# Kernel optimization log

Measured on AMD Instinct MI355X. Metric: run time of the kernel, lower is better.

## Reference

```python
import jax, jax.numpy as jnp
import numpy as np

NUM_ANCHORS = 3
NUM_CLASSES = 80


def setup_inputs() -> dict:
    key = jax.random.key(0)
    k1, _ = jax.random.split(key)
    B, C, G0, G1 = 16, NUM_ANCHORS * (NUM_CLASSES + 5), 64, 64
    x = jax.random.normal(k1, (B, C, G0, G1), dtype=jnp.float32)
    # normalized (w, h) anchor pairs, as in __init__
    anchors = jnp.array([[0.28, 0.22], [0.38, 0.48], [0.90, 0.78]], dtype=jnp.float32)
    return {"x": x, "anchors": anchors}


def reference(x, anchors):
    B = x.shape[0]
    A, nC = NUM_ANCHORS, NUM_CLASSES
    g0, g1 = x.shape[2], x.shape[3]
    # [B, A, g0, g1, 5+nC]
    pred = x.reshape(B, A, nC + 5, g0, g1).transpose(0, 1, 3, 4, 2)

    sx = jax.nn.sigmoid(pred[..., 0])
    sy = jax.nn.sigmoid(pred[..., 1])
    w = pred[..., 2]
    h = pred[..., 3]
    pred_conf = jax.nn.sigmoid(pred[..., 4])
    pred_cls = jax.nn.sigmoid(pred[..., 5:])

    # grid_x varies along axis 2 (row index), grid_y along axis 3 (col index),
    # matching the torch repeat/.t() construction in compute_grid_offsets.
    grid_x = jnp.arange(g0, dtype=x.dtype).reshape(1, 1, g0, 1)
    grid_y = jnp.arange(g1, dtype=x.dtype).reshape(1, 1, 1, g1)
    anchor_w = (anchors[:, 0] * g0).reshape(1, A, 1, 1)
    anchor_h = (anchors[:, 1] * g1).reshape(1, A, 1, 1)

    pred_boxes = jnp.stack(
        [
            sx + grid_x,
            sy + grid_y,
            jnp.exp(w) * anchor_w,
            jnp.exp(h) * anchor_h,
        ],
        axis=-1,
    )  # [B, A, g0, g1, 4]

    scale = jnp.array([g0, g1, g0, g1], dtype=x.dtype)
    return pred_boxes / scale, pred_conf, pred_cls
```

## Files before the change

kernel.cpp:

```cpp
#include <hip/hip_runtime.h>
#include <math.h>

#define NB 16
#define NA 3
#define NC 80
#define GS 4096
#define NPOS (NB * NA * GS)
#define STR 84

__device__ __forceinline__ float sigmoidf_(float v) {
    return 1.0f / (1.0f + __expf(-v));
}

__global__ __launch_bounds__(256, 7) void yolo_kernel(const float* __restrict__ x,
                                                      const float* __restrict__ anchors,
                                                      float* __restrict__ out) {
    __shared__ float lds[4][16 * STR];
    const int tid = threadIdx.x;
    const int w   = tid >> 6;
    const int l   = tid & 63;
    const int ba  = blockIdx.x >> 6;
    const int row = blockIdx.x & 63;
    const int s0  = (row << 6) + (w << 4);
    const float* __restrict__ xb = x + (size_t)ba * 85 * GS + s0;
    float* const ldsw = lds[w];

    const int chl = l >> 2;
    const int p4  = l & 3;
    const float* __restrict__ xc = xb + (size_t)(5 + chl) * GS + p4 * 4;

    float4 v[5];
    #pragma unroll
    for (int k = 0; k < 5; ++k)
        v[k] = *reinterpret_cast<const float4*>(xc + (size_t)k * 16 * GS);

    float tx = 0.f, ty = 0.f, tw = 0.f, th = 0.f, tc = 0.f;
    const bool box_lane = (l < 16);
    if (box_lane) {
        tx = xb[0 * GS + l];
        ty = xb[1 * GS + l];
        tw = xb[2 * GS + l];
        th = xb[3 * GS + l];
        tc = xb[4 * GS + l];
    }

    #pragma unroll
    for (int k = 0; k < 5; ++k) {
        #pragma unroll
        for (int j = 0; j < 4; ++j) {
            const float sv = sigmoidf_((&v[k].x)[j]);
            ldsw[(p4 * 4 + j) * STR + k * 16 + chl] = sv;
        }
    }

    if (box_lane) {
        const int p = s0 + l;
        const int t = ba * GS + p;
        const int a = ba % NA;
        float4 box;
        box.x = (sigmoidf_(tx) + (float)(p >> 6)) * (1.0f / 64.0f);
        box.y = (sigmoidf_(ty) + (float)(p & 63)) * (1.0f / 64.0f);
        box.z = __expf(tw) * anchors[a * 2 + 0];
        box.w = __expf(th) * anchors[a * 2 + 1];
        reinterpret_cast<float4*>(out)[t] = box;
        out[(size_t)NPOS * 4 + t] = sigmoidf_(tc);
    }

    float4* __restrict__ out4 =
        reinterpret_cast<float4*>(out + (size_t)NPOS * 5) + (size_t)(ba * GS + s0) * 20;
    #pragma unroll
    for (int k = 0; k < 5; ++k) {
        const int o4 = (k << 6) + l;
        const int o  = o4 << 2;
        const int p  = o / 80;
        const int ch = o - p * 80;
        out4[o4] = *reinterpret_cast<const float4*>(&ldsw[p * STR + ch]);
    }
}

extern "C" void kernel_launch(void* const* d_in, const int* in_sizes, int n_in,
                              void* d_out, int out_size, void* d_ws, size_t ws_size,
                              hipStream_t stream) {
    const float* x       = (const float*)d_in[0];
    const float* anchors = (const float*)d_in[1];
    float* out           = (float*)d_out;
    const int blocks = NB * NA * 64;
    yolo_kernel<<<blocks, 256, 0, stream>>>(x, anchors, out);
}
```

Baseline: 116.1 us.

## Use block-wide 128-position LDS transpose tile with channel-major layout

Each block now handles 128 spatial positions, where previously each wave handled its own 16-position slice. All 256 threads load class channels as float4 rows into a shared channel-major LDS tile padded to 133 floats per row. After a block barrier, the tile is read back position-major as scalar gathers and written out as float4. The grid shrinks by half and per-thread loads double. In exchange it adds a __syncthreads, and the minimum-occupancy hint in the launch bounds is dropped.

```diff
diff --git a/kernel.cpp b/kernel.cpp
--- a/kernel.cpp
+++ b/kernel.cpp
@@ -6,55 +6,43 @@
 #define NC 80
 #define GS 4096
 #define NPOS (NB * NA * GS)
-#define STR 84
+#define POSB 128
+#define LSTR 133
 
 __device__ __forceinline__ float sigmoidf_(float v) {
     return 1.0f / (1.0f + __expf(-v));
 }
 
-__global__ __launch_bounds__(256, 7) void yolo_kernel(const float* __restrict__ x,
-                                                      const float* __restrict__ anchors,
-                                                      float* __restrict__ out) {
-    __shared__ float lds[4][16 * STR];
-    const int tid = threadIdx.x;
-    const int w   = tid >> 6;
-    const int l   = tid & 63;
-    const int ba  = blockIdx.x >> 6;
-    const int row = blockIdx.x & 63;
-    const int s0  = (row << 6) + (w << 4);
+__global__ __launch_bounds__(256) void yolo_kernel(const float* __restrict__ x,
+                                                   const float* __restrict__ anchors,
+                                                   float* __restrict__ out) {
+    __shared__ float lds[NC * LSTR];
+    const int tid   = threadIdx.x;
+    const int ba    = blockIdx.x >> 5;
+    const int chunk = blockIdx.x & 31;
+    const int s0    = chunk << 7;
     const float* __restrict__ xb = x + (size_t)ba * 85 * GS + s0;
-    float* const ldsw = lds[w];
-
-    const int chl = l >> 2;
-    const int p4  = l & 3;
-    const float* __restrict__ xc = xb + (size_t)(5 + chl) * GS + p4 * 4;
-
-    float4 v[5];
-    #pragma unroll
-    for (int k = 0; k < 5; ++k)
-        v[k] = *reinterpret_cast<const float4*>(xc + (size_t)k * 16 * GS);
 
     float tx = 0.f, ty = 0.f, tw = 0.f, th = 0.f, tc = 0.f;
-    const bool box_lane = (l < 16);
+    const bool box_lane = (tid < POSB);
     if (box_lane) {
-        tx = xb[0 * GS + l];
-        ty = xb[1 * GS + l];
-        tw = xb[2 * GS + l];
-        th = xb[3 * GS + l];
-        tc = xb[4 * GS + l];
+        tx = xb[0 * GS + tid];
+        ty = xb[1 * GS + tid];
+        tw = xb[2 * GS + tid];
+        th = xb[3 * GS + tid];
+        tc = xb[4 * GS + tid];
     }
 
+    const int p4  = tid & 31;
+    const int chq = tid >> 5;
+    const float* __restrict__ xc = xb + (size_t)(5 + chq) * GS + p4 * 4;
+    float4 v[10];
     #pragma unroll
-    for (int k = 0; k < 5; ++k) {
-        #pragma unroll
-        for (int j = 0; j < 4; ++j) {
-            const float sv = sigmoidf_((&v[k].x)[j]);
-            ldsw[(p4 * 4 + j) * STR + k * 16 + chl] = sv;
-        }
-    }
+    for (int k = 0; k < 10; ++k)
+        v[k] = *reinterpret_cast<const float4*>(xc + (size_t)(8 * k) * GS);
 
     if (box_lane) {
-        const int p = s0 + l;
+        const int p = s0 + tid;
         const int t = ba * GS + p;
         const int a = ba % NA;
         float4 box;
@@ -66,15 +54,31 @@
         out[(size_t)NPOS * 4 + t] = sigmoidf_(tc);
     }
 
+    #pragma unroll
+    for (int k = 0; k < 10; ++k) {
+        const int ch = chq + 8 * k;
+        float* lr = &lds[ch * LSTR + p4 * 4];
+        lr[0] = sigmoidf_(v[k].x);
+        lr[1] = sigmoidf_(v[k].y);
+        lr[2] = sigmoidf_(v[k].z);
+        lr[3] = sigmoidf_(v[k].w);
+    }
+
+    __syncthreads();
+
     float4* __restrict__ out4 =
         reinterpret_cast<float4*>(out + (size_t)NPOS * 5) + (size_t)(ba * GS + s0) * 20;
     #pragma unroll
-    for (int k = 0; k < 5; ++k) {
-        const int o4 = (k << 6) + l;
-        const int o  = o4 << 2;
-        const int p  = o / 80;
-        const int ch = o - p * 80;
-        out4[o4] = *reinterpret_cast<const float4*>(&ldsw[p * STR + ch]);
+    for (int k = 0; k < 10; ++k) {
+        const int o4 = tid + (k << 8);
+        const int p  = o4 / 20;
+        const int c4 = o4 - p * 20;
+        float4 w4;
+        w4.x = lds[(c4 * 4 + 0) * LSTR + p];
+        w4.y = lds[(c4 * 4 + 1) * LSTR + p];
+        w4.z = lds[(c4 * 4 + 2) * LSTR + p];
+        w4.w = lds[(c4 * 4 + 3) * LSTR + p];
+        out4[o4] = w4;
     }
 }
 
@@ -84,6 +88,6 @@
     const float* x       = (const float*)d_in[0];
     const float* anchors = (const float*)d_in[1];
     float* out           = (float*)d_out;
-    const int blocks = NB * NA * 64;
+    const int blocks = NB * NA * 32;
     yolo_kernel<<<blocks, 256, 0, stream>>>(x, anchors, out);
 }
```

Result: faster. 112.6 us (median of 2 runs) (-3.0%).
